# Kernel tuning notes

Hardware: AMD Instinct MI355X
Metric: run time of the kernel (lower is better)

Reference implementation:

```python
import jax, jax.numpy as jnp
import numpy as np

B, S, D = 4, 4096, 1024

def setup_inputs() -> dict:
    key = jax.random.key(0)
    ks = jax.random.split(key, 5)
    scale = 1.0 / np.sqrt(D)
    return {
        "query": jax.random.normal(ks[0], (B, S, D), dtype=jnp.float32),
        "key": jax.random.normal(ks[1], (B, S, D), dtype=jnp.float32),
        "value": jax.random.normal(ks[2], (B, S, D), dtype=jnp.float32),
        "W": jax.random.normal(ks[3], (D, D), dtype=jnp.float32) * scale,  # torch Linear weight [out,in]
        "b": jax.random.normal(ks[4], (D,), dtype=jnp.float32) * 0.01,
    }

def reference(query, key, value, W, b):
    # shared projection (same_embd=True): q = Q W^T + b, same W,b for k,v
    q = jnp.einsum('bsd,od->bso', query, W) + b
    k = jnp.einsum('bsd,od->bso', key, W) + b
    v = jnp.einsum('bsd,od->bso', value, W) + b
    # unscaled dot-product attention (scaled=False default)
    a = jnp.einsum('bto,bso->bts', q, k)  # [B, tgt, src]
    attn = jax.nn.softmax(a, axis=2)
    output = jnp.einsum('bts,bso->bto', attn, v)
    return (output, attn)
```

## Files before the change

kernel.cpp:

```cpp
#include <hip/hip_runtime.h>
#include <hip/hip_bf16.h>
#include <hip/hip_fp16.h>

#define BD 4
#define SS 4096
#define DD 1024
#define RTOT (BD*SS)

typedef _Float16 f16;
typedef __attribute__((ext_vector_type(8))) _Float16 f16x8;
typedef __attribute__((ext_vector_type(4))) float f32x4;

static __device__ __forceinline__ unsigned short f2h(float f) {
  f16 h = (f16)f;
  return __builtin_bit_cast(unsigned short, h);
}
static __device__ __forceinline__ float h2f(unsigned short u) {
  return (float)__builtin_bit_cast(f16, u);
}

static __device__ __forceinline__ void gload16(const void* g, void* l) {
  __builtin_amdgcn_global_load_lds(
      (const __attribute__((address_space(1))) unsigned int*)g,
      (__attribute__((address_space(3))) unsigned int*)l, 16, 0, 0);
}

__global__ void split_w_kernel(const float* __restrict__ W,
                               unsigned short* __restrict__ Wh,
                               unsigned short* __restrict__ Wl) {
  int i = (blockIdx.x * 256 + threadIdx.x) * 4;
  float4 x = *reinterpret_cast<const float4*>(W + i);
  ushort4 h, l;
  h.x = f2h(x.x); l.x = f2h(x.x - h2f(h.x));
  h.y = f2h(x.y); l.y = f2h(x.y - h2f(h.y));
  h.z = f2h(x.z); l.z = f2h(x.z - h2f(h.z));
  h.w = f2h(x.w); l.w = f2h(x.w - h2f(h.w));
  *reinterpret_cast<ushort4*>(Wh + i) = h;
  *reinterpret_cast<ushort4*>(Wl + i) = l;
}

template<int TERMS, int EPI>
__global__ __launch_bounds__(512, 2)
void proj_one(const float* __restrict__ X,
              const unsigned short* __restrict__ Wh,
              const unsigned short* __restrict__ Wl,
              const float* __restrict__ bias,
              unsigned short* __restrict__ O1, unsigned short* __restrict__ O2)
{
  constexpr int OPS = 1 + TERMS;
  __shared__ unsigned short lds[2 * OPS][8192];
  const int tid = threadIdx.x, lane = tid & 63, wid = tid >> 6;
  const int t0 = blockIdx.x * 256;
  const int n0 = blockIdx.y * 256;

  const int sfr = (tid >> 2) & 15;
  const int scc = (tid & 3) ^ ((sfr >> 1) & 3);
  const int srowl = (tid >> 6) * 16 + sfr;
  const size_t arow0 = (size_t)(t0 + srowl) * DD;
  const size_t arow1 = (size_t)(t0 + srowl + 128) * DD;
  const size_t boff  = (size_t)(n0 + srowl) * DD + scc * 8;
  const int l0s = tid * 8;
  const int l1s = 4096 + tid * 8;

  float4 ar[4];

#define PBLOAD(cur, k0)  do { \
    gload16(Wh + boff + (k0),          &lds[(cur)*OPS+1][l0s]); \
    gload16(Wh + boff + 131072 + (k0), &lds[(cur)*OPS+1][l1s]); \
    if (TERMS == 2) { \
      gload16(Wl + boff + (k0),          &lds[(cur)*OPS+2][l0s]); \
      gload16(Wl + boff + 131072 + (k0), &lds[(cur)*OPS+2][l1s]); \
    } \
  } while (0)

#define PALOAD(k0) do { \
    ar[0] = *reinterpret_cast<const float4*>(X + arow0 + (k0) + scc * 8); \
    ar[1] = *reinterpret_cast<const float4*>(X + arow0 + (k0) + scc * 8 + 4); \
    ar[2] = *reinterpret_cast<const float4*>(X + arow1 + (k0) + scc * 8); \
    ar[3] = *reinterpret_cast<const float4*>(X + arow1 + (k0) + scc * 8 + 4); \
  } while (0)

#define PAWRITE(buf) do { \
    ushort4 u0, u1, u2, u3; \
    u0.x = f2h(ar[0].x); u0.y = f2h(ar[0].y); u0.z = f2h(ar[0].z); u0.w = f2h(ar[0].w); \
    u1.x = f2h(ar[1].x); u1.y = f2h(ar[1].y); u1.z = f2h(ar[1].z); u1.w = f2h(ar[1].w); \
    u2.x = f2h(ar[2].x); u2.y = f2h(ar[2].y); u2.z = f2h(ar[2].z); u2.w = f2h(ar[2].w); \
    u3.x = f2h(ar[3].x); u3.y = f2h(ar[3].y); u3.z = f2h(ar[3].z); u3.w = f2h(ar[3].w); \
    unsigned short* d0 = &lds[(buf)*OPS+0][l0s]; \
    *reinterpret_cast<ushort4*>(d0)     = u0; \
    *reinterpret_cast<ushort4*>(d0 + 4) = u1; \
    unsigned short* d1 = &lds[(buf)*OPS+0][l1s]; \
    *reinterpret_cast<ushort4*>(d1)     = u2; \
    *reinterpret_cast<ushort4*>(d1 + 4) = u3; \
  } while (0)

  const int wr = wid >> 2, wc = wid & 3;
  const int rfr = lane & 15, rcc = lane >> 4;
  const int lp8 = (rfr * 4 + (rcc ^ ((rfr >> 1) & 3))) * 8;

  f32x4 acc[8][4] = {};

  int cur = 0;
  PBLOAD(0, 0);
  PALOAD(0);
  PAWRITE(0);
  __syncthreads();

  for (int t = 0; t < 32; ++t) {
    if (t < 31) { PBLOAD(cur ^ 1, (t + 1) * 32); PALOAD((t + 1) * 32); }

    f16x8 bhf[4], blf[4];
#pragma unroll
    for (int n = 0; n < 4; ++n) {
      bhf[n] = *reinterpret_cast<const f16x8*>(&lds[cur * OPS + 1][(wc * 4 + n) * 512 + lp8]);
      if (TERMS == 2)
        blf[n] = *reinterpret_cast<const f16x8*>(&lds[cur * OPS + 2][(wc * 4 + n) * 512 + lp8]);
    }
#pragma unroll
    for (int h = 0; h < 2; ++h) {
      f16x8 ahf[4];
#pragma unroll
      for (int m = 0; m < 4; ++m)
        ahf[m] = *reinterpret_cast<const f16x8*>(&lds[cur * OPS + 0][(wr * 8 + h * 4 + m) * 512 + lp8]);
      __builtin_amdgcn_s_setprio(1);
#pragma unroll
      for (int m = 0; m < 4; ++m)
#pragma unroll
        for (int n = 0; n < 4; ++n) {
          acc[h * 4 + m][n] = __builtin_amdgcn_mfma_f32_16x16x32_f16(ahf[m], bhf[n], acc[h * 4 + m][n], 0, 0, 0);
          if (TERMS == 2)
            acc[h * 4 + m][n] = __builtin_amdgcn_mfma_f32_16x16x32_f16(ahf[m], blf[n], acc[h * 4 + m][n], 0, 0, 0);
        }
      __builtin_amdgcn_s_setprio(0);
    }

    if (t < 31) PAWRITE(cur ^ 1);
    __syncthreads();
    cur ^= 1;
  }
#undef PBLOAD
#undef PALOAD
#undef PAWRITE

  const int col = lane & 15, rb = (lane >> 4) * 4;
#pragma unroll
  for (int m = 0; m < 8; ++m)
#pragma unroll
    for (int n = 0; n < 4; ++n) {
      int oc = n0 + wc * 64 + n * 16 + col;
      float bv = bias[oc];
      if (EPI == 2) {
        int tr = t0 + wr * 128 + m * 16 + rb;
        int bb = tr >> 12, s = tr & (SS - 1);
        ushort4 h;
        h.x = f2h(acc[m][n][0] + bv);
        h.y = f2h(acc[m][n][1] + bv);
        h.z = f2h(acc[m][n][2] + bv);
        h.w = f2h(acc[m][n][3] + bv);
        *reinterpret_cast<ushort4*>(O1 + ((size_t)(bb * DD + oc)) * SS + s) = h;
      } else {
#pragma unroll
        for (int q = 0; q < 4; ++q) {
          int tr = t0 + wr * 128 + m * 16 + rb + q;
          float p = acc[m][n][q] + bv;
          if (EPI == 0) {
            O1[(size_t)tr * DD + oc] = f2h(p);
          } else {
            unsigned short h = f2h(p);
            O1[(size_t)tr * DD + oc] = h;
            O2[(size_t)tr * DD + oc] = f2h(p - h2f(h));
          }
        }
      }
    }
}

__global__ __launch_bounds__(512, 2)
void logits_v3(const unsigned short* __restrict__ qf,
               const unsigned short* __restrict__ kh, const unsigned short* __restrict__ kl,
               float* __restrict__ out)
{
  __shared__ unsigned short lds[6][8192];
  const int tid = threadIdx.x, lane = tid & 63, wid = tid >> 6;

  int bid = blockIdx.x;
  int swz = (bid & 7) * 128 + (bid >> 3);
  const int b = swz >> 8;
  const int r = swz & 255;
  const int t0 = (r >> 4) * 256, s0 = (r & 15) * 256;

  const unsigned short* qB  = qf + (size_t)b * SS * DD;
  const unsigned short* khB = kh + (size_t)b * SS * DD;
  const unsigned short* klB = kl + (size_t)b * SS * DD;

  const int sfr = (tid >> 2) & 15;
  const int scc = (tid & 3) ^ ((sfr >> 1) & 3);
  const int srowl = (tid >> 6) * 16 + sfr;
  const size_t qoff0 = (size_t)(t0 + srowl) * DD + scc * 8;
  const size_t koff0 = (size_t)(s0 + srowl) * DD + scc * 8;
  const int l0s = tid * 8;
  const int l1s = 4096 + tid * 8;

#define STAGE(cur, k0)  do { \
    gload16(qB  + qoff0 + (k0),          &lds[(cur)*3+0][l0s]); \
    gload16(qB  + qoff0 + 131072 + (k0), &lds[(cur)*3+0][l1s]); \
    gload16(khB + koff0 + (k0),          &lds[(cur)*3+1][l0s]); \
    gload16(khB + koff0 + 131072 + (k0), &lds[(cur)*3+1][l1s]); \
    gload16(klB + koff0 + (k0),          &lds[(cur)*3+2][l0s]); \
    gload16(klB + koff0 + 131072 + (k0), &lds[(cur)*3+2][l1s]); \
  } while (0)

  const int wr = wid >> 2, wc = wid & 3;
  const int rfr = lane & 15, rcc = lane >> 4;
  const int lp8 = (rfr * 4 + (rcc ^ ((rfr >> 1) & 3))) * 8;

  f32x4 acc[8][4] = {};

  int cur = 0;
  STAGE(0, 0);
  __syncthreads();

  for (int t = 0; t < 32; ++t) {
    if (t < 31) STAGE(cur ^ 1, (t + 1) * 32);

    f16x8 bhf[4], blf[4];
#pragma unroll
    for (int n = 0; n < 4; ++n) {
      bhf[n] = *reinterpret_cast<const f16x8*>(&lds[cur * 3 + 1][(wc * 4 + n) * 512 + lp8]);
      blf[n] = *reinterpret_cast<const f16x8*>(&lds[cur * 3 + 2][(wc * 4 + n) * 512 + lp8]);
    }
#pragma unroll
    for (int h = 0; h < 2; ++h) {
      f16x8 ahf[4];
#pragma unroll
      for (int m = 0; m < 4; ++m)
        ahf[m] = *reinterpret_cast<const f16x8*>(&lds[cur * 3 + 0][(wr * 8 + h * 4 + m) * 512 + lp8]);
      __builtin_amdgcn_s_setprio(1);
#pragma unroll
      for (int m = 0; m < 4; ++m)
#pragma unroll
        for (int n = 0; n < 4; ++n) {
          acc[h * 4 + m][n] = __builtin_amdgcn_mfma_f32_16x16x32_f16(ahf[m], bhf[n], acc[h * 4 + m][n], 0, 0, 0);
          acc[h * 4 + m][n] = __builtin_amdgcn_mfma_f32_16x16x32_f16(ahf[m], blf[n], acc[h * 4 + m][n], 0, 0, 0);
        }
      __builtin_amdgcn_s_setprio(0);
    }
    __syncthreads();
    cur ^= 1;
  }
#undef STAGE

  const int col = lane & 15, rb = (lane >> 4) * 4;
#pragma unroll
  for (int m = 0; m < 8; ++m)
#pragma unroll
    for (int n = 0; n < 4; ++n) {
      int s = s0 + wc * 64 + n * 16 + col;
#pragma unroll
      for (int q = 0; q < 4; ++q) {
        int tr = t0 + wr * 128 + m * 16 + rb + q;
        out[((size_t)b * SS + tr) * SS + s] = acc[m][n][q];
      }
    }
}

__global__ __launch_bounds__(256)
void softmax_kernel(float* __restrict__ attn) {
  float* rp = attn + (size_t)blockIdx.x * SS;
  const int tid = threadIdx.x, lane = tid & 63, wid = tid >> 6;
  float v[16];
  float m = -1e30f;
#pragma unroll
  for (int i = 0; i < 4; ++i) {
    float4 x = *reinterpret_cast<const float4*>(rp + i * 1024 + tid * 4);
    v[i * 4 + 0] = x.x; v[i * 4 + 1] = x.y; v[i * 4 + 2] = x.z; v[i * 4 + 3] = x.w;
    m = fmaxf(m, fmaxf(fmaxf(x.x, x.y), fmaxf(x.z, x.w)));
  }
#pragma unroll
  for (int off = 32; off; off >>= 1) m = fmaxf(m, __shfl_xor(m, off));
  __shared__ float redm[4], reds[4];
  if (lane == 0) redm[wid] = m;
  __syncthreads();
  m = fmaxf(fmaxf(redm[0], redm[1]), fmaxf(redm[2], redm[3]));
  float sum = 0.f;
#pragma unroll
  for (int i = 0; i < 16; ++i) { v[i] = __expf(v[i] - m); sum += v[i]; }
#pragma unroll
  for (int off = 32; off; off >>= 1) sum += __shfl_xor(sum, off);
  if (lane == 0) reds[wid] = sum;
  __syncthreads();
  float inv = 1.0f / (reds[0] + reds[1] + reds[2] + reds[3]);
#pragma unroll
  for (int i = 0; i < 4; ++i) {
    float4 x;
    x.x = v[i * 4 + 0] * inv; x.y = v[i * 4 + 1] * inv;
    x.z = v[i * 4 + 2] * inv; x.w = v[i * 4 + 3] * inv;
    *reinterpret_cast<float4*>(rp + i * 1024 + tid * 4) = x;
  }
}

__global__ __launch_bounds__(512)
void pv_v5(const float* __restrict__ attn, const unsigned short* __restrict__ vT,
           float* __restrict__ out)
{
  __shared__ unsigned short lds[8][8192];
  const int tid = threadIdx.x, lane = tid & 63, wid = tid >> 6;

  int bid = blockIdx.x;
  int swz = (bid & 7) * 32 + (bid >> 3);
  const int b = swz >> 6, rem = swz & 63;
  const int t0 = (rem >> 2) * 256;
  const int n0 = (rem & 3) * 256;
  const float* aB = attn + ((size_t)b * SS + t0) * SS;
  const unsigned short* vB = vT + ((size_t)b * DD + n0) * SS;

  const int sfr = (tid >> 2) & 15;
  const int scc = (tid & 3) ^ ((sfr >> 1) & 3);
  const int srowl = (tid >> 6) * 16 + sfr;
  const size_t row0 = (size_t)srowl * SS;
  const size_t row1 = (size_t)(srowl + 128) * SS;
  const int l0s = tid * 8, l1s = 4096 + tid * 8;

  const int wr = wid >> 2, wc = wid & 3;
  const int rfr = lane & 15, rcc = lane >> 4;
  const int lp8 = (rfr * 4 + (rcc ^ ((rfr >> 1) & 3))) * 8;

  f32x4 acc[8][4] = {};
  float4 ar[8];

#define PV5_BLOAD(buf, k0) do { \
    gload16(vB + row0 + (k0) + scc * 8,      &lds[(buf)*4+2][l0s]); \
    gload16(vB + row1 + (k0) + scc * 8,      &lds[(buf)*4+2][l1s]); \
    gload16(vB + row0 + (k0) + 32 + scc * 8, &lds[(buf)*4+3][l0s]); \
    gload16(vB + row1 + (k0) + 32 + scc * 8, &lds[(buf)*4+3][l1s]); \
  } while (0)

#define PV5_ALOAD(k0) do { \
    ar[0] = *reinterpret_cast<const float4*>(aB + row0 + (k0) + scc * 8); \
    ar[1] = *reinterpret_cast<const float4*>(aB + row0 + (k0) + scc * 8 + 4); \
    ar[2] = *reinterpret_cast<const float4*>(aB + row1 + (k0) + scc * 8); \
    ar[3] = *reinterpret_cast<const float4*>(aB + row1 + (k0) + scc * 8 + 4); \
    ar[4] = *reinterpret_cast<const float4*>(aB + row0 + (k0) + 32 + scc * 8); \
    ar[5] = *reinterpret_cast<const float4*>(aB + row0 + (k0) + 32 + scc * 8 + 4); \
    ar[6] = *reinterpret_cast<const float4*>(aB + row1 + (k0) + 32 + scc * 8); \
    ar[7] = *reinterpret_cast<const float4*>(aB + row1 + (k0) + 32 + scc * 8 + 4); \
  } while (0)

#define PV5_AWRITE(buf) do { \
    _Pragma("unroll") \
    for (int p = 0; p < 4; ++p) { \
      int s = p >> 1, hh = p & 1; \
      ushort4 u0, u1; \
      u0.x = f2h(ar[p*2].x);   u0.y = f2h(ar[p*2].y); \
      u0.z = f2h(ar[p*2].z);   u0.w = f2h(ar[p*2].w); \
      u1.x = f2h(ar[p*2+1].x); u1.y = f2h(ar[p*2+1].y); \
      u1.z = f2h(ar[p*2+1].z); u1.w = f2h(ar[p*2+1].w); \
      unsigned short* d = &lds[(buf)*4 + s][(hh ? l1s : l0s)]; \
      *reinterpret_cast<ushort4*>(d)     = u0; \
      *reinterpret_cast<ushort4*>(d + 4) = u1; \
    } \
  } while (0)

  int cur = 0;
  PV5_BLOAD(0, 0);
  PV5_ALOAD(0);
  PV5_AWRITE(0);
  __syncthreads();

  for (int it = 0; it < 64; ++it) {
    if (it < 63) { PV5_BLOAD(cur ^ 1, (it + 1) * 64); PV5_ALOAD((it + 1) * 64); }

#pragma unroll
    for (int s = 0; s < 2; ++s) {
      f16x8 bf[4];
#pragma unroll
      for (int n = 0; n < 4; ++n)
        bf[n] = *reinterpret_cast<const f16x8*>(&lds[cur * 4 + 2 + s][(wc * 4 + n) * 512 + lp8]);
#pragma unroll
      for (int h = 0; h < 2; ++h) {
        f16x8 af[4];
#pragma unroll
        for (int m = 0; m < 4; ++m)
          af[m] = *reinterpret_cast<const f16x8*>(&lds[cur * 4 + s][(wr * 8 + h * 4 + m) * 512 + lp8]);
        __builtin_amdgcn_s_setprio(1);
#pragma unroll
        for (int m = 0; m < 4; ++m)
#pragma unroll
          for (int n = 0; n < 4; ++n)
            acc[h * 4 + m][n] = __builtin_amdgcn_mfma_f32_16x16x32_f16(af[m], bf[n], acc[h * 4 + m][n], 0, 0, 0);
        __builtin_amdgcn_s_setprio(0);
      }
    }

    if (it < 63) PV5_AWRITE(cur ^ 1);
    __syncthreads();
    cur ^= 1;
  }
#undef PV5_BLOAD
#undef PV5_ALOAD
#undef PV5_AWRITE

  const int col = lane & 15, rb = (lane >> 4) * 4;
#pragma unroll
  for (int m = 0; m < 8; ++m)
#pragma unroll
    for (int n = 0; n < 4; ++n) {
      int o = n0 + wc * 64 + n * 16 + col;
#pragma unroll
      for (int q = 0; q < 4; ++q) {
        int t = t0 + wr * 128 + m * 16 + rb + q;
        out[((size_t)b * SS + t) * DD + o] = acc[m][n][q];
      }
    }
}

extern "C" void kernel_launch(void* const* d_in, const int* in_sizes, int n_in,
                              void* d_out, int out_size, void* d_ws, size_t ws_size,
                              hipStream_t stream) {
  const float* query = (const float*)d_in[0];
  const float* key   = (const float*)d_in[1];
  const float* value = (const float*)d_in[2];
  const float* W     = (const float*)d_in[3];
  const float* bias  = (const float*)d_in[4];

  float* out  = (float*)d_out;
  float* attn = out + (size_t)BD * SS * DD;

  unsigned short* Whf = (unsigned short*)d_ws;
  unsigned short* Wlf = Whf + (size_t)DD * DD;
  unsigned short* qfb = Wlf + (size_t)DD * DD;
  unsigned short* khi = qfb + (size_t)RTOT * DD;
  unsigned short* klo = khi + (size_t)RTOT * DD;
  unsigned short* vT  = klo + (size_t)RTOT * DD;

  split_w_kernel<<<DD * DD / (256 * 4), 256, 0, stream>>>(W, Whf, Wlf);

  dim3 gp(RTOT / 256, DD / 256);
  proj_one<2, 0><<<gp, 512, 0, stream>>>(query, Whf, Wlf, bias, qfb, nullptr);
  proj_one<2, 1><<<gp, 512, 0, stream>>>(key,   Whf, Wlf, bias, khi, klo);
  proj_one<1, 2><<<gp, 512, 0, stream>>>(value, Whf, nullptr, bias, vT, nullptr);

  logits_v3<<<(SS / 256) * (SS / 256) * BD, 512, 0, stream>>>(qfb, khi, klo, attn);
  softmax_kernel<<<RTOT, 256, 0, stream>>>(attn);
  pv_v5<<<(SS / 256) * (DD / 256) * BD, 512, 0, stream>>>(attn, vT, out);
}
```

Before: 698.9 us.

## Triple-buffer logits kernel LDS with two-stage prefetch and manual vmcnt waits

The QK logits kernel moves from double to triple LDS buffering, issuing global-to-LDS loads two K-steps ahead. The full __syncthreads is replaced by an explicit s_waitcnt vmcnt plus s_barrier, so loads for the next stage can stay in flight across the barrier. This aims to hide global memory latency behind the MFMA work. In exchange, LDS use rises to 144KB per block, which may limit occupancy.

Result: no change. 704.5 us (+0.8%).

```diff
diff --git a/kernel.cpp b/kernel.cpp
--- a/kernel.cpp
+++ b/kernel.cpp
@@ -176,11 +176,11 @@
 }
 
 __global__ __launch_bounds__(512, 2)
-void logits_v3(const unsigned short* __restrict__ qf,
+void logits_v4(const unsigned short* __restrict__ qf,
                const unsigned short* __restrict__ kh, const unsigned short* __restrict__ kl,
                float* __restrict__ out)
 {
-  __shared__ unsigned short lds[6][8192];
+  __shared__ unsigned short lds[9][8192];
   const int tid = threadIdx.x, lane = tid & 63, wid = tid >> 6;
 
   int bid = blockIdx.x;
@@ -201,13 +201,13 @@
   const int l0s = tid * 8;
   const int l1s = 4096 + tid * 8;
 
-#define STAGE(cur, k0)  do { \
-    gload16(qB  + qoff0 + (k0),          &lds[(cur)*3+0][l0s]); \
-    gload16(qB  + qoff0 + 131072 + (k0), &lds[(cur)*3+0][l1s]); \
-    gload16(khB + koff0 + (k0),          &lds[(cur)*3+1][l0s]); \
-    gload16(khB + koff0 + 131072 + (k0), &lds[(cur)*3+1][l1s]); \
-    gload16(klB + koff0 + (k0),          &lds[(cur)*3+2][l0s]); \
-    gload16(klB + koff0 + 131072 + (k0), &lds[(cur)*3+2][l1s]); \
+#define STAGE(buf, k0)  do { \
+    gload16(qB  + qoff0 + (k0),          &lds[(buf)*3+0][l0s]); \
+    gload16(qB  + qoff0 + 131072 + (k0), &lds[(buf)*3+0][l1s]); \
+    gload16(khB + koff0 + (k0),          &lds[(buf)*3+1][l0s]); \
+    gload16(khB + koff0 + 131072 + (k0), &lds[(buf)*3+1][l1s]); \
+    gload16(klB + koff0 + (k0),          &lds[(buf)*3+2][l0s]); \
+    gload16(klB + koff0 + 131072 + (k0), &lds[(buf)*3+2][l1s]); \
   } while (0)
 
   const int wr = wid >> 2, wc = wid & 3;
@@ -216,25 +216,30 @@
 
   f32x4 acc[8][4] = {};
 
-  int cur = 0;
   STAGE(0, 0);
-  __syncthreads();
-
+  STAGE(1, 32);
+  asm volatile("s_waitcnt vmcnt(6)" ::: "memory");
+  __builtin_amdgcn_s_barrier();
+
+  int cb = 0;
   for (int t = 0; t < 32; ++t) {
-    if (t < 31) STAGE(cur ^ 1, (t + 1) * 32);
+    if (t < 30) {
+      int pb = cb + 2; if (pb >= 3) pb -= 3;
+      STAGE(pb, (t + 2) * 32);
+    }
 
     f16x8 bhf[4], blf[4];
 #pragma unroll
     for (int n = 0; n < 4; ++n) {
-      bhf[n] = *reinterpret_cast<const f16x8*>(&lds[cur * 3 + 1][(wc * 4 + n) * 512 + lp8]);
-      blf[n] = *reinterpret_cast<const f16x8*>(&lds[cur * 3 + 2][(wc * 4 + n) * 512 + lp8]);
+      bhf[n] = *reinterpret_cast<const f16x8*>(&lds[cb * 3 + 1][(wc * 4 + n) * 512 + lp8]);
+      blf[n] = *reinterpret_cast<const f16x8*>(&lds[cb * 3 + 2][(wc * 4 + n) * 512 + lp8]);
     }
 #pragma unroll
     for (int h = 0; h < 2; ++h) {
       f16x8 ahf[4];
 #pragma unroll
       for (int m = 0; m < 4; ++m)
-        ahf[m] = *reinterpret_cast<const f16x8*>(&lds[cur * 3 + 0][(wr * 8 + h * 4 + m) * 512 + lp8]);
+        ahf[m] = *reinterpret_cast<const f16x8*>(&lds[cb * 3 + 0][(wr * 8 + h * 4 + m) * 512 + lp8]);
       __builtin_amdgcn_s_setprio(1);
 #pragma unroll
       for (int m = 0; m < 4; ++m)
@@ -245,8 +250,11 @@
         }
       __builtin_amdgcn_s_setprio(0);
     }
-    __syncthreads();
-    cur ^= 1;
+
+    if (t < 30)      asm volatile("s_waitcnt vmcnt(6)" ::: "memory");
+    else if (t == 30) asm volatile("s_waitcnt vmcnt(0)" ::: "memory");
+    __builtin_amdgcn_s_barrier();
+    cb = cb + 1; if (cb >= 3) cb -= 3;
   }
 #undef STAGE
 
@@ -440,7 +448,7 @@
   proj_one<2, 1><<<gp, 512, 0, stream>>>(key,   Whf, Wlf, bias, khi, klo);
   proj_one<1, 2><<<gp, 512, 0, stream>>>(value, Whf, nullptr, bias, vT, nullptr);
 
-  logits_v3<<<(SS / 256) * (SS / 256) * BD, 512, 0, stream>>>(qfb, khi, klo, attn);
+  logits_v4<<<(SS / 256) * (SS / 256) * BD, 512, 0, stream>>>(qfb, khi, klo, attn);
   softmax_kernel<<<RTOT, 256, 0, stream>>>(attn);
   pv_v5<<<(SS / 256) * (DD / 256) * BD, 512, 0, stream>>>(attn, vT, out);
 }
```

## Concatenate K hi/lo halves and rewrite logits GEMM with finer-grained pipelined LDS stages

Applied to the files above, without the earlier changes.

The key projection now writes its hi and lo fp16 parts into one buffer with 2048 columns per row, so the logits GEMM treats hi/lo as a doubled K dimension (K=2048) instead of issuing paired MFMAs on separate buffers. The logits kernel is rewritten with a 64-wide K step split into sub-stages, inline-asm LDS reads, explicit vmcnt/lgkmcnt waits and barriers interleaving global-to-LDS prefetch with MFMA phases. The goal is to keep more loads in flight and overlap memory with compute better. It adds hand-scheduled synchronisation that is fragile and depends on exact buffer indexing.

Measured after the change: 732.8 us. 4.8% more time.

```diff
diff --git a/kernel.cpp b/kernel.cpp
--- a/kernel.cpp
+++ b/kernel.cpp
@@ -167,8 +167,8 @@
             O1[(size_t)tr * DD + oc] = f2h(p);
           } else {
             unsigned short h = f2h(p);
-            O1[(size_t)tr * DD + oc] = h;
-            O2[(size_t)tr * DD + oc] = f2h(p - h2f(h));
+            O1[(size_t)tr * 2048 + oc] = h;
+            O1[(size_t)tr * 2048 + 1024 + oc] = f2h(p - h2f(h));
           }
         }
       }
@@ -176,11 +176,11 @@
 }
 
 __global__ __launch_bounds__(512, 2)
-void logits_v3(const unsigned short* __restrict__ qf,
-               const unsigned short* __restrict__ kh, const unsigned short* __restrict__ kl,
+void logits_v7(const unsigned short* __restrict__ qf,
+               const unsigned short* __restrict__ kc,
                float* __restrict__ out)
 {
-  __shared__ unsigned short lds[6][8192];
+  __shared__ unsigned short lds[65536];
   const int tid = threadIdx.x, lane = tid & 63, wid = tid >> 6;
 
   int bid = blockIdx.x;
@@ -190,65 +190,118 @@
   const int t0 = (r >> 4) * 256, s0 = (r & 15) * 256;
 
   const unsigned short* qB  = qf + (size_t)b * SS * DD;
-  const unsigned short* khB = kh + (size_t)b * SS * DD;
-  const unsigned short* klB = kl + (size_t)b * SS * DD;
+  const unsigned short* kcB = kc + (size_t)b * SS * 2048;
 
   const int sfr = (tid >> 2) & 15;
   const int scc = (tid & 3) ^ ((sfr >> 1) & 3);
   const int srowl = (tid >> 6) * 16 + sfr;
-  const size_t qoff0 = (size_t)(t0 + srowl) * DD + scc * 8;
-  const size_t koff0 = (size_t)(s0 + srowl) * DD + scc * 8;
-  const int l0s = tid * 8;
-  const int l1s = 4096 + tid * 8;
-
-#define STAGE(cur, k0)  do { \
-    gload16(qB  + qoff0 + (k0),          &lds[(cur)*3+0][l0s]); \
-    gload16(qB  + qoff0 + 131072 + (k0), &lds[(cur)*3+0][l1s]); \
-    gload16(khB + koff0 + (k0),          &lds[(cur)*3+1][l0s]); \
-    gload16(khB + koff0 + 131072 + (k0), &lds[(cur)*3+1][l1s]); \
-    gload16(klB + koff0 + (k0),          &lds[(cur)*3+2][l0s]); \
-    gload16(klB + koff0 + 131072 + (k0), &lds[(cur)*3+2][l1s]); \
+  const size_t qrow0 = (size_t)(t0 + srowl) * DD + scc * 8;
+  const size_t qrow1 = (size_t)(t0 + 128 + srowl) * DD + scc * 8;
+  const size_t krow0 = (size_t)(s0 + srowl) * 2048 + scc * 8;
+  const size_t krow1 = (size_t)(s0 + 128 + srowl) * 2048 + scc * 8;
+
+#define SG_A(TT, s, kk) do { \
+    gload16(qB + qrow0 + (kk), &lds[((TT)&1)*32768 + (s)*8192 +        tid*8]); \
+    gload16(qB + qrow1 + (kk), &lds[((TT)&1)*32768 + (s)*8192 + 4096 + tid*8]); \
+  } while (0)
+#define SG_B(TT, s, kk) do { \
+    gload16(kcB + krow0 + (kk), &lds[((TT)&1)*32768 + 16384 + (s)*8192 +        tid*8]); \
+    gload16(kcB + krow1 + (kk), &lds[((TT)&1)*32768 + 16384 + (s)*8192 + 4096 + tid*8]); \
   } while (0)
 
   const int wr = wid >> 2, wc = wid & 3;
   const int rfr = lane & 15, rcc = lane >> 4;
   const int lp8 = (rfr * 4 + (rcc ^ ((rfr >> 1) & 3))) * 8;
 
+  const unsigned ldsbase =
+      (unsigned)(size_t)(__attribute__((address_space(3))) unsigned short*)&lds[0];
+  const unsigned lane_off = (unsigned)(lp8 * 2);
+
   f32x4 acc[8][4] = {};
 
-  int cur = 0;
-  STAGE(0, 0);
-  __syncthreads();
-
-  for (int t = 0; t < 32; ++t) {
-    if (t < 31) STAGE(cur ^ 1, (t + 1) * 32);
-
-    f16x8 bhf[4], blf[4];
-#pragma unroll
-    for (int n = 0; n < 4; ++n) {
-      bhf[n] = *reinterpret_cast<const f16x8*>(&lds[cur * 3 + 1][(wc * 4 + n) * 512 + lp8]);
-      blf[n] = *reinterpret_cast<const f16x8*>(&lds[cur * 3 + 2][(wc * 4 + n) * 512 + lp8]);
-    }
-#pragma unroll
-    for (int h = 0; h < 2; ++h) {
-      f16x8 ahf[4];
-#pragma unroll
-      for (int m = 0; m < 4; ++m)
-        ahf[m] = *reinterpret_cast<const f16x8*>(&lds[cur * 3 + 0][(wr * 8 + h * 4 + m) * 512 + lp8]);
-      __builtin_amdgcn_s_setprio(1);
-#pragma unroll
-      for (int m = 0; m < 4; ++m)
-#pragma unroll
-        for (int n = 0; n < 4; ++n) {
-          acc[h * 4 + m][n] = __builtin_amdgcn_mfma_f32_16x16x32_f16(ahf[m], bhf[n], acc[h * 4 + m][n], 0, 0, 0);
-          acc[h * 4 + m][n] = __builtin_amdgcn_mfma_f32_16x16x32_f16(ahf[m], blf[n], acc[h * 4 + m][n], 0, 0, 0);
-        }
-      __builtin_amdgcn_s_setprio(0);
-    }
-    __syncthreads();
-    cur ^= 1;
+#define DSR(dst, addr) asm volatile("ds_read_b128 %0, %1" : "=&v"(dst) : "v"(addr))
+
+  SG_A(0, 0, 0);  SG_B(0, 0, 0);  SG_A(0, 1, 32); SG_B(0, 1, 32);
+  SG_B(1, 0, 64); SG_A(1, 0, 64); SG_B(1, 1, 96);
+  asm volatile("s_waitcnt vmcnt(6)" ::: "memory");
+  __builtin_amdgcn_s_barrier();
+
+  for (int T = 0; T < 32; ++T) {
+    const int c = T & 1;
+    const unsigned abase = ldsbase + lane_off + (unsigned)(c * 65536 + wr * 8192);
+    const unsigned bbase = ldsbase + lane_off +
+        (unsigned)(c * 65536 + 32768 + (wc >> 1) * 8192 + (wc & 1) * 4096);
+    f16x8 a0[4], a1[4], bf[4];
+
+#pragma unroll
+    for (int n = 0; n < 4; ++n) DSR(bf[n], bbase + (unsigned)(n * 1024));
+#pragma unroll
+    for (int m = 0; m < 4; ++m) DSR(a0[m], abase + (unsigned)(m * 1024));
+    if (T + 1 < 32) { int TT = T + 1; SG_A(TT, 1, (unsigned)((TT * 64 + 32) & 1023)); }
+    __builtin_amdgcn_s_barrier();
+    asm volatile("s_waitcnt lgkmcnt(0)" ::: "memory");
+    __builtin_amdgcn_sched_barrier(0);
+    __builtin_amdgcn_s_setprio(1);
+#pragma unroll
+    for (int m = 0; m < 4; ++m)
+#pragma unroll
+      for (int n = 0; n < 4; ++n)
+        acc[m][n] = __builtin_amdgcn_mfma_f32_16x16x32_f16(a0[m], bf[n], acc[m][n], 0, 0, 0);
+    __builtin_amdgcn_s_setprio(0);
+    __builtin_amdgcn_s_barrier();
+
+#pragma unroll
+    for (int m = 0; m < 4; ++m) DSR(a1[m], abase + (unsigned)((4 + m) * 1024));
+    if (T + 2 < 32) { int TT = T + 2; SG_B(TT, 0, (unsigned)(TT * 64)); }
+    __builtin_amdgcn_s_barrier();
+    asm volatile("s_waitcnt lgkmcnt(0)" ::: "memory");
+    __builtin_amdgcn_sched_barrier(0);
+    __builtin_amdgcn_s_setprio(1);
+#pragma unroll
+    for (int m = 0; m < 4; ++m)
+#pragma unroll
+      for (int n = 0; n < 4; ++n)
+        acc[4 + m][n] = __builtin_amdgcn_mfma_f32_16x16x32_f16(a1[m], bf[n], acc[4 + m][n], 0, 0, 0);
+    __builtin_amdgcn_s_setprio(0);
+    __builtin_amdgcn_s_barrier();
+
+#pragma unroll
+    for (int n = 0; n < 4; ++n) DSR(bf[n], bbase + (unsigned)(16384 + n * 1024));
+#pragma unroll
+    for (int m = 0; m < 4; ++m) DSR(a0[m], abase + (unsigned)(16384 + m * 1024));
+    if (T + 2 < 32) { int TT = T + 2; SG_A(TT, 0, (unsigned)((TT * 64) & 1023)); }
+    __builtin_amdgcn_s_barrier();
+    asm volatile("s_waitcnt lgkmcnt(0)" ::: "memory");
+    __builtin_amdgcn_sched_barrier(0);
+    __builtin_amdgcn_s_setprio(1);
+#pragma unroll
+    for (int m = 0; m < 4; ++m)
+#pragma unroll
+      for (int n = 0; n < 4; ++n)
+        acc[m][n] = __builtin_amdgcn_mfma_f32_16x16x32_f16(a0[m], bf[n], acc[m][n], 0, 0, 0);
+    __builtin_amdgcn_s_setprio(0);
+    __builtin_amdgcn_s_barrier();
+
+#pragma unroll
+    for (int m = 0; m < 4; ++m) DSR(a1[m], abase + (unsigned)(16384 + (4 + m) * 1024));
+    if (T + 2 < 32) { int TT = T + 2; SG_B(TT, 1, (unsigned)(TT * 64 + 32)); }
+    __builtin_amdgcn_s_barrier();
+    asm volatile("s_waitcnt lgkmcnt(0)" ::: "memory");
+    __builtin_amdgcn_sched_barrier(0);
+    __builtin_amdgcn_s_setprio(1);
+#pragma unroll
+    for (int m = 0; m < 4; ++m)
+#pragma unroll
+      for (int n = 0; n < 4; ++n)
+        acc[4 + m][n] = __builtin_amdgcn_mfma_f32_16x16x32_f16(a1[m], bf[n], acc[4 + m][n], 0, 0, 0);
+    __builtin_amdgcn_s_setprio(0);
+    if (T < 30) asm volatile("s_waitcnt vmcnt(6)" ::: "memory");
+    else        asm volatile("s_waitcnt vmcnt(0)" ::: "memory");
+    __builtin_amdgcn_s_barrier();
   }
-#undef STAGE
+#undef SG_A
+#undef SG_B
+#undef DSR
 
   const int col = lane & 15, rb = (lane >> 4) * 4;
 #pragma unroll
@@ -429,18 +482,17 @@
   unsigned short* Whf = (unsigned short*)d_ws;
   unsigned short* Wlf = Whf + (size_t)DD * DD;
   unsigned short* qfb = Wlf + (size_t)DD * DD;
-  unsigned short* khi = qfb + (size_t)RTOT * DD;
-  unsigned short* klo = khi + (size_t)RTOT * DD;
-  unsigned short* vT  = klo + (size_t)RTOT * DD;
+  unsigned short* kc  = qfb + (size_t)RTOT * DD;
+  unsigned short* vT  = kc  + (size_t)RTOT * 2048;
 
   split_w_kernel<<<DD * DD / (256 * 4), 256, 0, stream>>>(W, Whf, Wlf);
 
   dim3 gp(RTOT / 256, DD / 256);
   proj_one<2, 0><<<gp, 512, 0, stream>>>(query, Whf, Wlf, bias, qfb, nullptr);
-  proj_one<2, 1><<<gp, 512, 0, stream>>>(key,   Whf, Wlf, bias, khi, klo);
+  proj_one<2, 1><<<gp, 512, 0, stream>>>(key,   Whf, Wlf, bias, kc,  nullptr);
   proj_one<1, 2><<<gp, 512, 0, stream>>>(value, Whf, nullptr, bias, vT, nullptr);
 
-  logits_v3<<<(SS / 256) * (SS / 256) * BD, 512, 0, stream>>>(qfb, khi, klo, attn);
+  logits_v7<<<(SS / 256) * (SS / 256) * BD, 512, 0, stream>>>(qfb, kc, attn);
   softmax_kernel<<<RTOT, 256, 0, stream>>>(attn);
   pv_v5<<<(SS / 256) * (DD / 256) * BD, 512, 0, stream>>>(attn, vT, out);
 }
```
